# Performance work log

Measured on AMD Instinct MI355X. Metric: run time of the kernel, lower is better.

The kernel has to match this reference:

```python
import jax, jax.numpy as jnp
import numpy as np

N_BLOCKS = 8
BLOCK_C = 32  # 256 channels / 8 blocks


def setup_inputs() -> dict:
    key = jax.random.key(0)
    k1, k2 = jax.random.split(key)
    x = jax.random.normal(k1, (16, 256, 128, 128), dtype=jnp.float32)
    # per-block invertible 1x1 conv weights (random Gaussian is invertible a.s.)
    w = jax.random.normal(k2, (N_BLOCKS, BLOCK_C, BLOCK_C), dtype=jnp.float32)
    logdet = jnp.zeros((16,), dtype=jnp.float32)
    return {"x": x, "w": w, "logdet": logdet}


def reference(x, w, logdet):
    # NOTE: the original forward calls self.perm(z, reverse) but discards the
    # result, so the channel shuffle has no effect on the output; we match that.
    B, C, H, W = x.shape
    nb, c, _ = w.shape
    # block-diagonal 1x1 conv == batched matmul over channel sub-blocks
    xb = x.reshape(B, nb, c, H, W)
    zb = jnp.einsum('kdc,bkchw->bkdhw', w, xb)
    z = zb.reshape(B, C, H, W)
    # dlogdet = sum over blocks of slogdet(W_k) * pixels
    _, ld = jnp.linalg.slogdet(w)            # [nb]
    dlogdet = jnp.sum(ld) * (H * W)
    return z, logdet + dlogdet
```

## Files before the change

kernel.cpp:

```cpp
#include <hip/hip_runtime.h>
#include <math.h>

#define HW    16384
#define NB    8
#define BC    32
#define BATCH 16
#define Z_ELEMS (16 * 256 * HW)

typedef float v4f __attribute__((ext_vector_type(4)));

__global__ __launch_bounds__(256) void conv_kernel(const float* __restrict__ x,
                                                   const float* __restrict__ w,
                                                   float* __restrict__ out) {
    const int tid = threadIdx.x;
    const int blk = blockIdx.x;
    const int s   = blk >> 4;
    const int k   = s & 7;
    const int pix = ((blk & 15) << 10) + (tid << 2);

    const size_t base = (size_t)s * (BC * HW);
    const float* xp = x   + base + pix;
    float*       op = out + base + pix;
    const float* wk = w + k * (BC * BC);

    v4f acc[BC];
#pragma unroll
    for (int d = 0; d < BC; ++d) acc[d] = (v4f)(0.f);

    v4f cur0 = __builtin_nontemporal_load((const v4f*)(xp));
    v4f cur1 = __builtin_nontemporal_load((const v4f*)(xp + HW));

    for (int c = 0; c < BC; c += 2) {
        v4f nxt0 = (v4f)(0.f), nxt1 = (v4f)(0.f);
        if (c + 2 < BC) {
            nxt0 = __builtin_nontemporal_load((const v4f*)(xp + (size_t)(c + 2) * HW));
            nxt1 = __builtin_nontemporal_load((const v4f*)(xp + (size_t)(c + 3) * HW));
        }
#pragma unroll
        for (int d = 0; d < BC; ++d) {
            const float w0 = wk[d * BC + c];
            const float w1 = wk[d * BC + c + 1];
            acc[d] += w0 * cur0;
            acc[d] += w1 * cur1;
        }
        cur0 = nxt0;
        cur1 = nxt1;
    }

#pragma unroll
    for (int d = 0; d < BC; ++d) {
        __builtin_nontemporal_store(acc[d], (v4f*)(op + (size_t)d * HW));
    }
}

__global__ __launch_bounds__(512) void logdet_kernel(const float* __restrict__ w,
                                                     const float* __restrict__ ld_in,
                                                     float* __restrict__ out) {
    __shared__ float m[NB][BC][BC + 1];
    __shared__ float ldpart[NB];

    const int tid  = threadIdx.x;
    const int wv   = tid >> 6;
    const int lane = tid & 63;

    for (int idx = lane; idx < BC * BC; idx += 64)
        m[wv][idx >> 5][idx & 31] = w[wv * BC * BC + idx];
    __syncthreads();

    float ldsum = 0.f;
    for (int kk = 0; kk < BC; ++kk) {
        int p = kk;
        if (lane == 0) {
            float best = fabsf(m[wv][kk][kk]);
            for (int i = kk + 1; i < BC; ++i) {
                float v = fabsf(m[wv][i][kk]);
                if (v > best) { best = v; p = i; }
            }
        }
        p = __shfl(p, 0);

        if (p != kk && lane < BC) {
            float t         = m[wv][kk][lane];
            m[wv][kk][lane] = m[wv][p][lane];
            m[wv][p][lane]  = t;
        }
        __syncthreads();

        const float pivot = m[wv][kk][kk];
        ldsum += logf(fabsf(pivot));

        if (lane > kk && lane < BC) {
            const float f = m[wv][lane][kk] / pivot;
            for (int j = kk + 1; j < BC; ++j)
                m[wv][lane][j] -= f * m[wv][kk][j];
        }
        __syncthreads();
    }

    if (lane == 0) ldpart[wv] = ldsum;
    __syncthreads();

    if (tid < BATCH) {
        float tot = 0.f;
#pragma unroll
        for (int i = 0; i < NB; ++i) tot += ldpart[i];
        out[Z_ELEMS + tid] = ld_in[tid] + tot * (float)HW;
    }
}

extern "C" void kernel_launch(void* const* d_in, const int* in_sizes, int n_in,
                              void* d_out, int out_size, void* d_ws, size_t ws_size,
                              hipStream_t stream) {
    const float* x  = (const float*)d_in[0];
    const float* w  = (const float*)d_in[1];
    const float* ld = (const float*)d_in[2];
    float* out = (float*)d_out;

    conv_kernel<<<dim3(2048), dim3(256), 0, stream>>>(x, w, out);
    logdet_kernel<<<dim3(1), dim3(512), 0, stream>>>(w, ld, out);
}
```

Before: 504.0 us.

## Fuse logdet into conv kernel using register-resident shuffle-based LU

The separate single-block logdet kernel is folded into the conv launch as an extra block 0, removing one kernel launch and its serialization after the conv. The LU factorization is rewritten to keep one matrix row per lane in registers, using cross-lane shuffles for pivot search and row broadcast instead of shared memory with block-wide barriers. Each wave handles two matrices in its two 32-lane halves. Block 0 runs the serial LU while the other blocks do the conv, so the logdet work overlaps with the bandwidth-bound main work.

Measured after the change: 429.0 us (median of 2 runs). 1.17x faster.

```diff
diff --git a/kernel.cpp b/kernel.cpp
--- a/kernel.cpp
+++ b/kernel.cpp
@@ -9,11 +9,72 @@
 
 typedef float v4f __attribute__((ext_vector_type(4)));
 
-__global__ __launch_bounds__(256) void conv_kernel(const float* __restrict__ x,
-                                                   const float* __restrict__ w,
-                                                   float* __restrict__ out) {
+__global__ __launch_bounds__(256) void fused_kernel(const float* __restrict__ x,
+                                                    const float* __restrict__ w,
+                                                    const float* __restrict__ ld_in,
+                                                    float* __restrict__ out) {
+    if (blockIdx.x == 0) {
+        const int tid  = threadIdx.x;
+        const int wv   = tid >> 6;
+        const int lane = tid & 63;
+        const int row  = lane & 31;
+        const int mi   = (wv << 1) | (lane >> 5);
+
+        float r[BC];
+        {
+            const float* wr = w + mi * (BC * BC) + row * BC;
+            const v4f* wr4 = (const v4f*)wr;
+#pragma unroll
+            for (int j4 = 0; j4 < BC / 4; ++j4) {
+                v4f v = wr4[j4];
+                r[j4 * 4 + 0] = v.x;
+                r[j4 * 4 + 1] = v.y;
+                r[j4 * 4 + 2] = v.z;
+                r[j4 * 4 + 3] = v.w;
+            }
+        }
+
+        float ldsum  = 0.f;
+        bool  active = true;
+
+#pragma unroll
+        for (int t = 0; t < BC; ++t) {
+            float cand = active ? fabsf(r[t]) : -1.0f;
+            int   idx  = row;
+#pragma unroll
+            for (int off = 1; off < 32; off <<= 1) {
+                float oc = __shfl_xor(cand, off);
+                int   oi = __shfl_xor(idx, off);
+                if (oc > cand || (oc == cand && oi < idx)) { cand = oc; idx = oi; }
+            }
+            const int   plane = (lane & 32) | idx;
+            const float pv    = __shfl(r[t], plane);
+            ldsum += logf(cand);
+
+            const float f = (active && lane != plane) ? (r[t] / pv) : 0.0f;
+#pragma unroll
+            for (int j = t + 1; j < BC; ++j) {
+                const float pj = __shfl(r[j], plane);
+                r[j] = fmaf(-f, pj, r[j]);
+            }
+            if (lane == plane) active = false;
+        }
+
+        __shared__ float ldpart[NB];
+        if (row == 0) ldpart[mi] = ldsum;
+        __syncthreads();
+
+        if (tid < BATCH) {
+            float tot = 0.f;
+#pragma unroll
+            for (int i = 0; i < NB; ++i) tot += ldpart[i];
+            out[Z_ELEMS + tid] = ld_in[tid] + tot * (float)HW;
+        }
+        return;
+    }
+
     const int tid = threadIdx.x;
-    const int blk = blockIdx.x;
+    const int blk = blockIdx.x - 1;
     const int s   = blk >> 4;
     const int k   = s & 7;
     const int pix = ((blk & 15) << 10) + (tid << 2);
@@ -53,61 +114,6 @@
     }
 }
 
-__global__ __launch_bounds__(512) void logdet_kernel(const float* __restrict__ w,
-                                                     const float* __restrict__ ld_in,
-                                                     float* __restrict__ out) {
-    __shared__ float m[NB][BC][BC + 1];
-    __shared__ float ldpart[NB];
-
-    const int tid  = threadIdx.x;
-    const int wv   = tid >> 6;
-    const int lane = tid & 63;
-
-    for (int idx = lane; idx < BC * BC; idx += 64)
-        m[wv][idx >> 5][idx & 31] = w[wv * BC * BC + idx];
-    __syncthreads();
-
-    float ldsum = 0.f;
-    for (int kk = 0; kk < BC; ++kk) {
-        int p = kk;
-        if (lane == 0) {
-            float best = fabsf(m[wv][kk][kk]);
-            for (int i = kk + 1; i < BC; ++i) {
-                float v = fabsf(m[wv][i][kk]);
-                if (v > best) { best = v; p = i; }
-            }
-        }
-        p = __shfl(p, 0);
-
-        if (p != kk && lane < BC) {
-            float t         = m[wv][kk][lane];
-            m[wv][kk][lane] = m[wv][p][lane];
-            m[wv][p][lane]  = t;
-        }
-        __syncthreads();
-
-        const float pivot = m[wv][kk][kk];
-        ldsum += logf(fabsf(pivot));
-
-        if (lane > kk && lane < BC) {
-            const float f = m[wv][lane][kk] / pivot;
-            for (int j = kk + 1; j < BC; ++j)
-                m[wv][lane][j] -= f * m[wv][kk][j];
-        }
-        __syncthreads();
-    }
-
-    if (lane == 0) ldpart[wv] = ldsum;
-    __syncthreads();
-
-    if (tid < BATCH) {
-        float tot = 0.f;
-#pragma unroll
-        for (int i = 0; i < NB; ++i) tot += ldpart[i];
-        out[Z_ELEMS + tid] = ld_in[tid] + tot * (float)HW;
-    }
-}
-
 extern "C" void kernel_launch(void* const* d_in, const int* in_sizes, int n_in,
                               void* d_out, int out_size, void* d_ws, size_t ws_size,
                               hipStream_t stream) {
@@ -116,6 +122,5 @@
     const float* ld = (const float*)d_in[2];
     float* out = (float*)d_out;
 
-    conv_kernel<<<dim3(2048), dim3(256), 0, stream>>>(x, w, out);
-    logdet_kernel<<<dim3(1), dim3(512), 0, stream>>>(w, ld, out);
+    fused_kernel<<<dim3(2049), dim3(256), 0, stream>>>(x, w, ld, out);
 }
```
